# Optimization experiments

Measured on AMD Instinct MI355X. Metric: run time of the kernel, lower is better.

Reference implementation:

```python
import jax, jax.numpy as jnp
import numpy as np

V = 32000   # vocab
D = 1024    # dim
H = 16      # query heads
HKV = 8     # kv heads (GQA)
DH = D // H # head dim = 64
L = 2       # layers
FF = 3584   # expert hidden dim
E = 8       # experts
K = 2       # top-k
EPS = 1e-5
BASE = 1000000.0
B, S = 1, 2048


def setup_inputs() -> dict:
    key = jax.random.key(0)
    ks = jax.random.split(key, 10)
    s = 0.02
    return {
        "x": jax.random.randint(ks[0], (B, S), 0, V, dtype=jnp.int64) if jax.config.jax_enable_x64 else jax.random.randint(ks[0], (B, S), 0, V),
        "emb": jax.random.normal(ks[1], (V, D), jnp.float32) * s,
        "ln_w": jnp.ones((L, D), jnp.float32),
        "ffln_w": jnp.ones((L, D), jnp.float32),
        "wq": jax.random.normal(ks[2], (L, D, H * DH), jnp.float32) * s,
        "wk": jax.random.normal(ks[3], (L, D, HKV * DH), jnp.float32) * s,
        "wv": jax.random.normal(ks[4], (L, D, HKV * DH), jnp.float32) * s,
        "wo": jax.random.normal(ks[5], (L, H * DH, D), jnp.float32) * s,
        "gate_w": jax.random.normal(ks[6], (L, E, D), jnp.float32) * s,
        "w1": jax.random.normal(ks[7], (L, E, FF, D), jnp.float32) * s,
        "w2": jax.random.normal(ks[8], (L, E, D, FF), jnp.float32) * s,
        "w3": jax.random.normal(ks[9], (L, E, FF, D), jnp.float32) * s,
        "dec_norm_w": jnp.ones((D,), jnp.float32),
    }


def rmsnorm(x, w):
    # LayerNormParameterized(use_mean=False, shift=False) == RMSNorm, pow in fp32
    xf = x.astype(jnp.float32)
    var = jnp.mean(xf * xf, axis=-1, keepdims=True)
    return ((xf * jax.lax.rsqrt(var + EPS)).astype(x.dtype)) * w


def rope(xh, pos):
    # interleaved (complex-pair) rotary embedding, xh: [B, S, h, DH]
    half = DH // 2
    freqs = 1.0 / (BASE ** (jnp.arange(0, half, dtype=jnp.float32) * 2.0 / DH))
    ang = pos[:, None] * freqs[None, :]                       # [S, half]
    cos = jnp.cos(ang)[None, :, None, :]
    sin = jnp.sin(ang)[None, :, None, :]
    x1 = xh[..., 0::2]
    x2 = xh[..., 1::2]
    out = jnp.stack([x1 * cos - x2 * sin, x1 * sin + x2 * cos], axis=-1)
    return out.reshape(xh.shape)


def reference(x, emb, ln_w, ffln_w, wq, wk, wv, wo, gate_w, w1, w2, w3, dec_norm_w):
    h = emb[x]                                                # [B, S, D]
    pos = jnp.arange(S, dtype=jnp.float32)
    causal = jnp.tril(jnp.ones((S, S), bool))[None, None]     # [1,1,S,S]
    scale = 1.0 / np.sqrt(DH).astype(np.float32)
    for i in range(L):
        # --- attention sub-layer ---
        res = h
        xn = rmsnorm(h, ln_w[i])
        q = rope((xn @ wq[i]).reshape(B, S, H, DH), pos)
        k = rope((xn @ wk[i]).reshape(B, S, HKV, DH), pos)
        v = (xn @ wv[i]).reshape(B, S, HKV, DH)
        rep = H // HKV
        k = jnp.repeat(k, rep, axis=2)                        # [B,S,H,DH]
        v = jnp.repeat(v, rep, axis=2)
        scores = jnp.einsum('bqhd,bkhd->bhqk', q, k) * scale
        scores = jnp.where(causal, scores, jnp.float32(-1e9))
        att = jax.nn.softmax(scores, axis=-1)
        o = jnp.einsum('bhqk,bkhd->bqhd', att, v).reshape(B, S, H * DH) @ wo[i]
        h = res + o
        # --- MoE FFN sub-layer ---
        res = h
        xn = rmsnorm(h, ffln_w[i]).reshape(B * S, D)          # [T, D]
        logits = xn @ gate_w[i].T                             # [T, E]
        gates = jax.nn.softmax(logits, axis=-1)
        topw, topi = jax.lax.top_k(gates, K)                  # [T, K]
        topw = topw / jnp.sum(topw, axis=-1, keepdims=True)
        # dense combine weights [T, E] (zero for unselected experts)
        cw = jnp.einsum('tk,tke->te', topw, jax.nn.one_hot(topi, E, dtype=topw.dtype))
        y = jnp.zeros_like(xn)
        for e in range(E):                                    # fixed small expert loop
            ye = (jax.nn.silu(xn @ w1[i, e].T) * (xn @ w3[i, e].T)) @ w2[i, e].T
            y = y + cw[:, e:e + 1] * ye
        h = res + y.reshape(B, S, D)
    return rmsnorm(h, dec_norm_w)
```

## Files before the change

### kernel.cpp

```cpp
#include <hip/hip_runtime.h>

using u16 = unsigned short;
using u32 = unsigned int;

#define TT 2048
#define DM 1024
#define NH 16
#define NKV 8
#define DHD 64
#define FFD 3584
#define NE 8

typedef __bf16 bf16x8 __attribute__((ext_vector_type(8)));
typedef float f32x4 __attribute__((ext_vector_type(4)));

__device__ __forceinline__ u16 f2bf(float x){
  return __builtin_bit_cast(u16, (__bf16)x);
}
__device__ __forceinline__ float bf2f(u16 h){
  return (float)__builtin_bit_cast(__bf16, h);
}
__device__ __forceinline__ f32x4 mfma16(bf16x8 a, bf16x8 b, f32x4 c){
  return __builtin_amdgcn_mfma_f32_16x16x32_bf16(a, b, c, 0, 0, 0);
}
__device__ __forceinline__ uint4 packhi8v(float4 a, float4 b){
  u16 h0=f2bf(a.x),h1=f2bf(a.y),h2=f2bf(a.z),h3=f2bf(a.w);
  u16 h4=f2bf(b.x),h5=f2bf(b.y),h6=f2bf(b.z),h7=f2bf(b.w);
  return make_uint4((u32)h0|((u32)h1<<16),(u32)h2|((u32)h3<<16),
                    (u32)h4|((u32)h5<<16),(u32)h6|((u32)h7<<16));
}
__device__ __forceinline__ uint4 packlo8v(float4 a, float4 b){
  u16 l0=f2bf(a.x-bf2f(f2bf(a.x))),l1=f2bf(a.y-bf2f(f2bf(a.y)));
  u16 l2=f2bf(a.z-bf2f(f2bf(a.z))),l3=f2bf(a.w-bf2f(f2bf(a.w)));
  u16 l4=f2bf(b.x-bf2f(f2bf(b.x))),l5=f2bf(b.y-bf2f(f2bf(b.y)));
  u16 l6=f2bf(b.z-bf2f(f2bf(b.z))),l7=f2bf(b.w-bf2f(f2bf(b.w)));
  return make_uint4((u32)l0|((u32)l1<<16),(u32)l2|((u32)l3<<16),
                    (u32)l4|((u32)l5<<16),(u32)l6|((u32)l7<<16));
}

#define SWC(r,c) ((((c) ^ ((((r)>>1) ^ ((r)>>3)) & 3))) * 8)

__global__ __launch_bounds__(256) void k_embed(const int* __restrict__ x,
    const float* __restrict__ emb, float* __restrict__ h){
  int t = blockIdx.x;
  int d = threadIdx.x * 4;
  float4 v = *reinterpret_cast<const float4*>(emb + (size_t)x[t] * DM + d);
  *reinterpret_cast<float4*>(h + (size_t)t * DM + d) = v;
}

template<int OUTF32>
__global__ __launch_bounds__(256) void k_rmsnorm(const float* __restrict__ in,
    const float* __restrict__ w, u16* __restrict__ oh, u16* __restrict__ ol,
    float* __restrict__ of){
  int t = blockIdx.x;
  int d4 = threadIdx.x * 4;
  float4 xv = *reinterpret_cast<const float4*>(in + (size_t)t * DM + d4);
  float ss = xv.x*xv.x + xv.y*xv.y + xv.z*xv.z + xv.w*xv.w;
#pragma unroll
  for (int m = 1; m < 64; m <<= 1) ss += __shfl_xor(ss, m);
  __shared__ float sred[4];
  if ((threadIdx.x & 63) == 0) sred[threadIdx.x >> 6] = ss;
  __syncthreads();
  float tot = sred[0] + sred[1] + sred[2] + sred[3];
  float r = 1.0f / sqrtf(tot * (1.0f / DM) + 1e-5f);
  float vv[4] = {xv.x, xv.y, xv.z, xv.w};
#pragma unroll
  for (int jj = 0; jj < 4; jj++){
    float xn = (vv[jj] * r) * w[d4 + jj];
    size_t a = (size_t)t * DM + d4 + jj;
    if constexpr (OUTF32){
      of[a] = xn;
    } else {
      u16 hi = f2bf(xn);
      oh[a] = hi;
      ol[a] = f2bf(xn - bf2f(hi));
    }
  }
}

template<int NHD>
__global__ __launch_bounds__(256) void k_rope(const float* __restrict__ in,
    u16* __restrict__ oh, u16* __restrict__ ol){
  int idx = blockIdx.x * 256 + threadIdx.x;
  int j = idx & 31;
  int hd = (idx >> 5) % NHD;
  int s = idx / (32 * NHD);
  size_t base = ((size_t)s * NHD + hd) * 64 + 2 * j;
  float x1 = in[base], x2 = in[base + 1];
  float xe = (float)j * 0.03125f;
  float yf = (float)pow(1.0e6, (double)xe);
  float fr = 1.0f / yf;
  float ang = (float)s * fr;
  double ad = (double)ang;
  float c  = (float)cos(ad);
  float sn = (float)sin(ad);
  float o1 = x1 * c - x2 * sn;
  float o2 = x1 * sn + x2 * c;
  u16 h1 = f2bf(o1), h2 = f2bf(o2);
  oh[base]     = h1; ol[base]     = f2bf(o1 - bf2f(h1));
  oh[base + 1] = h2; ol[base + 1] = f2bf(o2 - bf2f(h2));
}

__global__ __launch_bounds__(256) void k_splitbuf(const float* __restrict__ in,
    u16* __restrict__ oh, u16* __restrict__ ol, int n){
  int i = blockIdx.x * 256 + threadIdx.x;
  if (i < n){
    float x = in[i];
    u16 hi = f2bf(x);
    oh[i] = hi;
    ol[i] = f2bf(x - bf2f(hi));
  }
}

__global__ __launch_bounds__(256) void k_gate(const u16* __restrict__ xh,
    const u16* __restrict__ xl, const float* __restrict__ gw,
    int* __restrict__ topi, float* __restrict__ topw, int* __restrict__ cnt){
  int wv = threadIdx.x >> 6, lane = threadIdx.x & 63;
  int t = blockIdx.x * 4 + wv;
  float x[16];
#pragma unroll
  for (int i = 0; i < 16; i++){
    size_t a = (size_t)t * DM + lane + 64 * i;
    x[i] = bf2f(xh[a]) + bf2f(xl[a]);
  }
  float lgt[8];
#pragma unroll
  for (int e = 0; e < 8; e++){
    float s = 0.f;
#pragma unroll
    for (int i = 0; i < 16; i++) s += x[i] * gw[(size_t)e * DM + lane + 64 * i];
#pragma unroll
    for (int m = 1; m < 64; m <<= 1) s += __shfl_xor(s, m);
    lgt[e] = s;
  }
  float mx = lgt[0];
#pragma unroll
  for (int e = 1; e < 8; e++) mx = fmaxf(mx, lgt[e]);
  float p[8]; float sum = 0.f;
#pragma unroll
  for (int e = 0; e < 8; e++){ p[e] = expf(lgt[e] - mx); sum += p[e]; }
  float g[8];
#pragma unroll
  for (int e = 0; e < 8; e++) g[e] = p[e] / sum;
  int t0 = 0; float b0 = g[0];
#pragma unroll
  for (int e = 1; e < 8; e++) if (g[e] > b0){ b0 = g[e]; t0 = e; }
  int t1 = -1; float b1 = -1.f;
#pragma unroll
  for (int e = 0; e < 8; e++) if (e != t0 && g[e] > b1){ b1 = g[e]; t1 = e; }
  float ssum = b0 + b1;
  float w0 = b0 / ssum, w1 = b1 / ssum;
  if (lane == 0 && t < TT){
    topi[2*t] = t0; topi[2*t+1] = t1;
    topw[2*t] = w0; topw[2*t+1] = w1;
    atomicAdd(&cnt[t0], 1);
    atomicAdd(&cnt[t1], 1);
  }
}

__global__ void k_zero8(int* cnt){ if (threadIdx.x < 8) cnt[threadIdx.x] = 0; }

__global__ void k_scan(const int* __restrict__ cnt, int* __restrict__ offp, int* __restrict__ cur){
  if (threadIdx.x == 0){
    int r = 0;
    for (int e = 0; e < 8; e++){ offp[e] = r; r += cnt[e]; }
  }
  if (threadIdx.x < 8) cur[threadIdx.x] = 0;
}

__global__ __launch_bounds__(256) void k_scatter(const int* __restrict__ topi,
    const float* __restrict__ topw, const int* __restrict__ offp, int* __restrict__ cur,
    int* __restrict__ ftok, float* __restrict__ fwt){
  int t = blockIdx.x * 256 + threadIdx.x;
  if (t < TT){
#pragma unroll
    for (int j = 0; j < 2; j++){
      int e = topi[2*t + j];
      int p = atomicAdd(&cur[e], 1);
      ftok[offp[e] + p] = t;
      fwt[offp[e] + p] = topw[2*t + j];
    }
  }
}

#define GPRELOAD(KK) do { \
    pAh0 = *reinterpret_cast<const uint4*>(Ah + arowA0 + (KK)); \
    pAh1 = *reinterpret_cast<const uint4*>(Ah + arowA1 + (KK)); \
    if constexpr (SPLIT){ \
      pAl0 = *reinterpret_cast<const uint4*>(Al + arowA0 + (KK)); \
      pAl1 = *reinterpret_cast<const uint4*>(Al + arowA1 + (KK)); \
    } \
    if constexpr (BLAYOUT == 0){ \
      const float* bp_ = Bw + (size_t)(n0 + br0) * K + (KK) + cb8; \
      pB0 = *reinterpret_cast<const float4*>(bp_); \
      pB1 = *reinterpret_cast<const float4*>(bp_ + 4); \
      if constexpr (TN == 128){ \
        const float* bp2_ = Bw + (size_t)(n0 + br1) * K + (KK) + cb8; \
        pB2 = *reinterpret_cast<const float4*>(bp2_); \
        pB3 = *reinterpret_cast<const float4*>(bp2_ + 4); \
      } \
      if constexpr (DUAL){ \
        const float* bq_ = B3w + (size_t)(n0 + br0) * K + (KK) + cb8; \
        pB2 = *reinterpret_cast<const float4*>(bq_); \
        pB3 = *reinterpret_cast<const float4*>(bq_ + 4); \
      } \
    } else { \
      pB0 = *reinterpret_cast<const float4*>(Bw + (size_t)((KK) + kk1) * Nq + n0 + nn1); \
      pB1 = *reinterpret_cast<const float4*>(Bw + (size_t)((KK) + 16 + kk1) * Nq + n0 + nn1); \
    } \
  } while(0)

template<int BLAYOUT, int EPI, int SPLIT, int DUAL, int TN, int KS>
__global__ __launch_bounds__(256) void k_gemm(
    const u16* __restrict__ Ah, const u16* __restrict__ Al,
    const float* __restrict__ Bw, const float* __restrict__ B3w,
    const float* __restrict__ Bw2, const float* __restrict__ Bw3,
    size_t strideB, int N, int K,
    float* __restrict__ Cf, int ldc,
    float* __restrict__ Cf2, float* __restrict__ Cf3,
    u16* __restrict__ Ch, u16* __restrict__ Cl,
    const int* __restrict__ cntp, const int* __restrict__ offp,
    const int* __restrict__ ftok, const float* __restrict__ fwt)
{
  static_assert(!(DUAL && TN != 64), "DUAL uses TN=64");
  static_assert(!(BLAYOUT == 1 && TN != 64), "BLAYOUT=1 uses TN=64");
  int cnt = TT, off = 0, ks = 0;
  if constexpr (EPI == 2 || EPI == 3){
    int e = blockIdx.z / KS;
    ks = blockIdx.z % KS;
    cnt = cntp[e]; off = offp[e];
    if ((int)blockIdx.y * 128 >= cnt) return;
    Bw += (size_t)e * strideB;
    if constexpr (DUAL) B3w += (size_t)e * strideB;
  } else if constexpr (KS > 1){
    ks = blockIdx.z;
  }
  __shared__ u16 Ash[128][32];
  __shared__ u16 Asl[SPLIT ? 128 : 1][32];
  __shared__ u16 Bh1[TN][32];
  __shared__ u16 Bl1[SPLIT ? TN : 1][32];
  __shared__ u16 Bh3[DUAL ? TN : 1][32];
  __shared__ u16 Bl3[(DUAL && SPLIT) ? TN : 1][32];

  const int tid = threadIdx.x;
  const int m0 = blockIdx.y * 128;

  int n0, Nq = N, ldq = ldc;
  float* Cq = Cf;
  if constexpr (EPI == 4){
    int bx = blockIdx.x;
    if (bx < 16){       n0 = bx * 64;        Nq = 1024; ldq = 1024; Cq = Cf;  }
    else if (bx < 24){  n0 = (bx - 16) * 64; Nq = 512;  ldq = 512;  Cq = Cf2; Bw = Bw2; }
    else {              n0 = (bx - 24) * 64; Nq = 512;  ldq = 512;  Cq = Cf3; Bw = Bw3; }
  } else {
    n0 = blockIdx.x * TN;
  }

  const int r0 = tid >> 2;
  const int r1 = r0 + 64;
  const int ca = tid & 3;
  const int ca8 = ca * 8;
  int gr0, gr1;
  {
    int g0 = m0 + r0, g1 = m0 + r1;
    if constexpr (EPI == 2){
      gr0 = ftok[off + (g0 < cnt ? g0 : cnt - 1)];
      gr1 = ftok[off + (g1 < cnt ? g1 : cnt - 1)];
    } else if constexpr (EPI == 3){
      gr0 = off + (g0 < cnt ? g0 : cnt - 1);
      gr1 = off + (g1 < cnt ? g1 : cnt - 1);
    } else {
      gr0 = g0; gr1 = g1;
    }
  }
  const size_t arowA0 = (size_t)gr0 * K + ca8;
  const size_t arowA1 = (size_t)gr1 * K + ca8;
  const int swA0 = SWC(r0, ca), swA1 = SWC(r1, ca);

  const int br0 = tid >> 2;
  const int br1 = br0 + 64;
  const int cb8 = (tid & 3) * 8;
  const int swB0 = SWC(br0, tid & 3), swB1 = SWC(br1, tid & 3);
  const int kk1 = tid >> 4;
  const int nn1 = (tid & 15) * 4;

  const int wid = tid >> 6, lane = tid & 63;
  const int wr = wid >> 1, wc = wid & 1;
  const int lr = lane & 15, lg = lane >> 4;
  constexpr int NF = TN / 32;

  f32x4 acc[4][NF];
  f32x4 acc3[DUAL ? 4 : 1][NF];
#pragma unroll
  for (int m = 0; m < 4; m++)
#pragma unroll
    for (int n = 0; n < NF; n++){
      acc[m][n] = f32x4{0.f,0.f,0.f,0.f};
      if constexpr (DUAL) acc3[m][n] = f32x4{0.f,0.f,0.f,0.f};
    }

  uint4 pAh0, pAh1, pAl0{}, pAl1{};
  float4 pB0{}, pB1{}, pB2{}, pB3{};

  const int kbeg = ks * (K / KS);
  const int kend = kbeg + (K / KS);

  GPRELOAD(kbeg);
  for (int k0 = kbeg; k0 < kend; k0 += 32){
    *reinterpret_cast<uint4*>(&Ash[r0][swA0]) = pAh0;
    *reinterpret_cast<uint4*>(&Ash[r1][swA1]) = pAh1;
    if constexpr (SPLIT){
      *reinterpret_cast<uint4*>(&Asl[r0][swA0]) = pAl0;
      *reinterpret_cast<uint4*>(&Asl[r1][swA1]) = pAl1;
    }
    if constexpr (BLAYOUT == 0){
      *reinterpret_cast<uint4*>(&Bh1[br0][swB0]) = packhi8v(pB0, pB1);
      if constexpr (SPLIT) *reinterpret_cast<uint4*>(&Bl1[br0][swB0]) = packlo8v(pB0, pB1);
      if constexpr (TN == 128){
        *reinterpret_cast<uint4*>(&Bh1[br1][swB1]) = packhi8v(pB2, pB3);
        if constexpr (SPLIT) *reinterpret_cast<uint4*>(&Bl1[br1][swB1]) = packlo8v(pB2, pB3);
      }
      if constexpr (DUAL){
        *reinterpret_cast<uint4*>(&Bh3[br0][swB0]) = packhi8v(pB2, pB3);
        if constexpr (SPLIT) *reinterpret_cast<uint4*>(&Bl3[br0][swB0]) = packlo8v(pB2, pB3);
      }
    } else {
      const float* q0 = reinterpret_cast<const float*>(&pB0);
      const float* q1 = reinterpret_cast<const float*>(&pB1);
      const int ch0 = kk1 >> 3, off0 = kk1 & 7;
#pragma unroll
      for (int j = 0; j < 4; j++){
        int row = nn1 + j;
        int c0 = SWC(row, ch0) + off0;
        int c1 = SWC(row, ch0 + 2) + off0;
        u16 h0 = f2bf(q0[j]);
        Bh1[row][c0] = h0;
        if constexpr (SPLIT) Bl1[row][c0] = f2bf(q0[j] - bf2f(h0));
        u16 h1 = f2bf(q1[j]);
        Bh1[row][c1] = h1;
        if constexpr (SPLIT) Bl1[row][c1] = f2bf(q1[j] - bf2f(h1));
      }
    }
    __syncthreads();
    if (k0 + 32 < kend){ GPRELOAD(k0 + 32); }

    bf16x8 af[4], afl[4];
#pragma unroll
    for (int m = 0; m < 4; m++){
      int Ra = wr*64 + m*16 + lr;
      int sa = SWC(Ra, lg);
      af[m] = *reinterpret_cast<const bf16x8*>(&Ash[Ra][sa]);
      if constexpr (SPLIT)
        afl[m] = *reinterpret_cast<const bf16x8*>(&Asl[Ra][sa]);
    }
#pragma unroll
    for (int n = 0; n < NF; n++){
      int Rb = wc*(TN/2) + n*16 + lr;
      int sb = SWC(Rb, lg);
      bf16x8 b1 = *reinterpret_cast<const bf16x8*>(&Bh1[Rb][sb]);
#pragma unroll
      for (int m = 0; m < 4; m++) acc[m][n] = mfma16(af[m], b1, acc[m][n]);
      if constexpr (SPLIT){
        bf16x8 bl = *reinterpret_cast<const bf16x8*>(&Bl1[Rb][sb]);
#pragma unroll
        for (int m = 0; m < 4; m++){
          acc[m][n] = mfma16(af[m], bl, acc[m][n]);
          acc[m][n] = mfma16(afl[m], b1, acc[m][n]);
        }
      }
      if constexpr (DUAL){
        bf16x8 b3 = *reinterpret_cast<const bf16x8*>(&Bh3[Rb][sb]);
#pragma unroll
        for (int m = 0; m < 4; m++) acc3[m][n] = mfma16(af[m], b3, acc3[m][n]);
        if constexpr (SPLIT){
          bf16x8 b3l = *reinterpret_cast<const bf16x8*>(&Bl3[Rb][sb]);
#pragma unroll
          for (int m = 0; m < 4; m++){
            acc3[m][n] = mfma16(af[m], b3l, acc3[m][n]);
            acc3[m][n] = mfma16(afl[m], b3, acc3[m][n]);
          }
        }
      }
    }
    __syncthreads();
  }

#pragma unroll
  for (int m = 0; m < 4; m++)
#pragma unroll
    for (int n = 0; n < NF; n++)
#pragma unroll
      for (int r = 0; r < 4; r++){
        int row = m0 + wr*64 + m*16 + lg*4 + r;
        int col = n0 + wc*(TN/2) + n*16 + lr;
        float v = acc[m][n][r];
        if constexpr (EPI == 0){
          Cf[(size_t)row * ldc + col] = v;
        } else if constexpr (EPI == 1){
          if constexpr (KS > 1) atomicAdd(&Cf[(size_t)row * ldc + col], v);
          else                  Cf[(size_t)row * ldc + col] += v;
        } else if constexpr (EPI == 2){
          if (row < cnt){
            float a3 = acc3[m][n][r];
            float s = v / (1.0f + expf(-v));
            float y = s * a3;
            u16 hi = f2bf(y);
            size_t oa = (size_t)(off + row) * ldc + col;
            Ch[oa] = hi;
            Cl[oa] = f2bf(y - bf2f(hi));
          }
        } else if constexpr (EPI == 3){
          if (row < cnt){
            int tok = ftok[off + row];
            float wgt = fwt[off + row];
            atomicAdd(&Cf[(size_t)tok * ldc + col], wgt * v);
          }
        } else {
          if constexpr (KS > 1) atomicAdd(&Cq[(size_t)row * ldq + col], v);
          else                  Cq[(size_t)row * ldq + col] = v;
        }
      }
}

__global__ __launch_bounds__(256) void k_attn(
    const u16* __restrict__ qh, const u16* __restrict__ ql,
    const u16* __restrict__ kh, const u16* __restrict__ kl,
    const u16* __restrict__ vh, const u16* __restrict__ vl,
    u16* __restrict__ aoh, u16* __restrict__ aol)
{
  const int h  = blockIdx.y;
  const int q0 = blockIdx.x * 64;
  const int hk = h >> 1;
  const int tid = threadIdx.x;
  const int wv = tid >> 6, lane = tid & 63;
  const int lr = lane & 15, lg = lane >> 4;
  const int qw0 = q0 + wv * 16;

  __shared__ u16 Khs[32][72], Kls[32][72];
  __shared__ u16 Vhs[64][40], Vls[64][40];
  __shared__ u16 Phs[4][16][40], Pls[4][16][40];

  bf16x8 qfh[2], qfl[2];
#pragma unroll
  for (int dc = 0; dc < 2; dc++){
    size_t qa = ((size_t)(qw0 + lr) * NH + h) * 64 + dc*32 + lg*8;
    qfh[dc] = *reinterpret_cast<const bf16x8*>(qh + qa);
    qfl[dc] = *reinterpret_cast<const bf16x8*>(ql + qa);
  }
  f32x4 oacc[4];
  float mrun[4], lrun[4];
#pragma unroll
  for (int r = 0; r < 4; r++){ mrun[r] = -1e30f; lrun[r] = 0.f; }
#pragma unroll
  for (int g = 0; g < 4; g++) oacc[g] = f32x4{0.f,0.f,0.f,0.f};

  const int nt = q0 / 32 + 2;
  for (int kt = 0; kt < nt; kt++){
    int kg = kt * 32;
    {
      int kk = tid >> 3, c8 = (tid & 7) * 8;
      size_t ka = ((size_t)(kg + kk) * NKV + hk) * 64 + c8;
      *reinterpret_cast<uint4*>(&Khs[kk][c8]) = *reinterpret_cast<const uint4*>(kh + ka);
      *reinterpret_cast<uint4*>(&Kls[kk][c8]) = *reinterpret_cast<const uint4*>(kl + ka);
      uint4 v1 = *reinterpret_cast<const uint4*>(vh + ka);
      uint4 v2 = *reinterpret_cast<const uint4*>(vl + ka);
      const u16* p1 = reinterpret_cast<const u16*>(&v1);
      const u16* p2 = reinterpret_cast<const u16*>(&v2);
#pragma unroll
      for (int j = 0; j < 8; j++){ Vhs[c8 + j][kk] = p1[j]; Vls[c8 + j][kk] = p2[j]; }
    }
    __syncthreads();

    f32x4 sc[2];
    sc[0] = f32x4{0.f,0.f,0.f,0.f};
    sc[1] = f32x4{0.f,0.f,0.f,0.f};
#pragma unroll
    for (int c = 0; c < 2; c++){
#pragma unroll
      for (int dc = 0; dc < 2; dc++){
        bf16x8 bh = *reinterpret_cast<const bf16x8*>(&Khs[c*16 + lr][dc*32 + lg*8]);
        bf16x8 bl = *reinterpret_cast<const bf16x8*>(&Kls[c*16 + lr][dc*32 + lg*8]);
        sc[c] = mfma16(qfh[dc], bh, sc[c]);
        sc[c] = mfma16(qfh[dc], bl, sc[c]);
        sc[c] = mfma16(qfl[dc], bh, sc[c]);
      }
    }
    float pnew[2][4], corr[4];
#pragma unroll
    for (int r = 0; r < 4; r++){
      int row = qw0 + lg*4 + r;
      float s0 = (kg + lr      <= row) ? sc[0][r] * 0.125f : -1e30f;
      float s1 = (kg + 16 + lr <= row) ? sc[1][r] * 0.125f : -1e30f;
      float tm = fmaxf(s0, s1);
#pragma unroll
      for (int m = 1; m < 16; m <<= 1) tm = fmaxf(tm, __shfl_xor(tm, m));
      float mnew = fmaxf(mrun[r], tm);
      corr[r] = expf(mrun[r] - mnew);
      float p0 = expf(s0 - mnew);
      float p1 = expf(s1 - mnew);
      pnew[0][r] = p0; pnew[1][r] = p1;
      float sm = p0 + p1;
#pragma unroll
      for (int m = 1; m < 16; m <<= 1) sm += __shfl_xor(sm, m);
      lrun[r] = lrun[r] * corr[r] + sm;
      mrun[r] = mnew;
    }
#pragma unroll
    for (int g = 0; g < 4; g++){
      f32x4 t = oacc[g];
#pragma unroll
      for (int r = 0; r < 4; r++) t[r] *= corr[r];
      oacc[g] = t;
    }
#pragma unroll
    for (int c = 0; c < 2; c++)
#pragma unroll
      for (int r = 0; r < 4; r++){
        float p = pnew[c][r];
        u16 hi = f2bf(p);
        Phs[wv][lg*4 + r][c*16 + lr] = hi;
        Pls[wv][lg*4 + r][c*16 + lr] = f2bf(p - bf2f(hi));
      }
    asm volatile("s_waitcnt lgkmcnt(0)" ::: "memory");
    __builtin_amdgcn_sched_barrier(0);
    bf16x8 pah = *reinterpret_cast<const bf16x8*>(&Phs[wv][lr][lg*8]);
    bf16x8 pal = *reinterpret_cast<const bf16x8*>(&Pls[wv][lr][lg*8]);
#pragma unroll
    for (int g = 0; g < 4; g++){
      bf16x8 vb1 = *reinterpret_cast<const bf16x8*>(&Vhs[g*16 + lr][lg*8]);
      bf16x8 vb2 = *reinterpret_cast<const bf16x8*>(&Vls[g*16 + lr][lg*8]);
      oacc[g] = mfma16(pah, vb1, oacc[g]);
      oacc[g] = mfma16(pah, vb2, oacc[g]);
      oacc[g] = mfma16(pal, vb1, oacc[g]);
    }
    __syncthreads();
  }
#pragma unroll
  for (int g = 0; g < 4; g++)
#pragma unroll
    for (int r = 0; r < 4; r++){
      int row = qw0 + lg*4 + r;
      float v = oacc[g][r] / lrun[r];
      u16 hi = f2bf(v);
      size_t oa = ((size_t)row * NH + h) * 64 + g*16 + lr;
      aoh[oa] = hi;
      aol[oa] = f2bf(v - bf2f(hi));
    }
}

extern "C" void kernel_launch(void* const* d_in, const int* in_sizes, int n_in,
                              void* d_out, int out_size, void* d_ws, size_t ws_size,
                              hipStream_t stream){
  const int*   x     = (const int*)d_in[0];
  const float* emb   = (const float*)d_in[1];
  const float* lnw   = (const float*)d_in[2];
  const float* fflnw = (const float*)d_in[3];
  const float* wq    = (const float*)d_in[4];
  const float* wk    = (const float*)d_in[5];
  const float* wvp   = (const float*)d_in[6];
  const float* wo    = (const float*)d_in[7];
  const float* gw    = (const float*)d_in[8];
  const float* w1    = (const float*)d_in[9];
  const float* w2    = (const float*)d_in[10];
  const float* w3    = (const float*)d_in[11];
  const float* dnw   = (const float*)d_in[12];
  float* out = (float*)d_out;

  char* p = (char*)d_ws;
  auto alloc = [&](size_t bytes)->char*{
    char* r = p; p += (bytes + 255) & ~(size_t)255; return r;
  };
  float* h    = (float*)alloc((size_t)TT * DM * 4);
  float* qbuf = (float*)alloc((size_t)TT * 1024 * 4);
  float* kbuf = (float*)alloc((size_t)TT * 512 * 4);
  float* vbuf = (float*)alloc((size_t)TT * 512 * 4);
  u16* xnh = (u16*)alloc((size_t)TT * DM * 2);
  u16* xnl = (u16*)alloc((size_t)TT * DM * 2);
  u16* qhb = (u16*)alloc((size_t)TT * 1024 * 2);
  u16* qlb = (u16*)alloc((size_t)TT * 1024 * 2);
  u16* khb = (u16*)alloc((size_t)TT * 512 * 2);
  u16* klb = (u16*)alloc((size_t)TT * 512 * 2);
  u16* vhb = (u16*)alloc((size_t)TT * 512 * 2);
  u16* vlb = (u16*)alloc((size_t)TT * 512 * 2);
  u16* aoh = (u16*)alloc((size_t)TT * 1024 * 2);
  u16* aol = (u16*)alloc((size_t)TT * 1024 * 2);
  u16* acth = (u16*)alloc((size_t)2 * TT * FFD * 2);
  u16* actl = (u16*)alloc((size_t)2 * TT * FFD * 2);
  int*   topi = (int*)alloc((size_t)2 * TT * 4);
  float* topw = (float*)alloc((size_t)2 * TT * 4);
  int* cnt  = (int*)alloc(64);
  int* offe = (int*)alloc(64);
  int* cur  = (int*)alloc(64);
  int*   ftok = (int*)alloc((size_t)2 * TT * 4);
  float* fwt  = (float*)alloc((size_t)2 * TT * 4);

  k_embed<<<TT, 256, 0, stream>>>(x, emb, h);

  for (int i = 0; i < 2; i++){
    const float* wq_i = wq + (size_t)i * DM * 1024;
    const float* wk_i = wk + (size_t)i * DM * 512;
    const float* wv_i = wvp + (size_t)i * DM * 512;
    const float* wo_i = wo + (size_t)i * 1024 * DM;
    const float* w1_i = w1 + (size_t)i * NE * FFD * DM;
    const float* w2_i = w2 + (size_t)i * NE * DM * FFD;
    const float* w3_i = w3 + (size_t)i * NE * FFD * DM;

    k_rmsnorm<0><<<TT, 256, 0, stream>>>(h, lnw + i * DM, xnh, xnl, nullptr);

    hipMemsetAsync(qbuf, 0, (size_t)TT * 1024 * 4, stream);
    hipMemsetAsync(kbuf, 0, (size_t)TT * 512 * 4, stream);
    hipMemsetAsync(vbuf, 0, (size_t)TT * 512 * 4, stream);
    k_gemm<1,4,1,0,64,2><<<dim3(32,16,2), 256, 0, stream>>>(xnh, xnl,
        wq_i, nullptr, wk_i, wv_i, 0, 1024, DM,
        qbuf, 1024, kbuf, vbuf, nullptr, nullptr, nullptr, nullptr, nullptr, nullptr);

    k_rope<16><<<4096, 256, 0, stream>>>(qbuf, qhb, qlb);
    k_rope<8><<<2048, 256, 0, stream>>>(kbuf, khb, klb);
    k_splitbuf<<<4096, 256, 0, stream>>>(vbuf, vhb, vlb, TT * 512);

    k_attn<<<dim3(32,16,1), 256, 0, stream>>>(qhb, qlb, khb, klb, vhb, vlb, aoh, aol);

    k_gemm<1,1,1,0,64,2><<<dim3(16,16,2), 256, 0, stream>>>(aoh, aol,
        wo_i, nullptr, nullptr, nullptr, 0, DM, 1024,
        h, DM, nullptr, nullptr, nullptr, nullptr, nullptr, nullptr, nullptr, nullptr);

    k_rmsnorm<0><<<TT, 256, 0, stream>>>(h, fflnw + i * DM, xnh, xnl, nullptr);

    k_zero8<<<1, 64, 0, stream>>>(cnt);
    k_gate<<<TT/4, 256, 0, stream>>>(xnh, xnl, gw + (size_t)i * NE * DM, topi, topw, cnt);
    k_scan<<<1, 64, 0, stream>>>(cnt, offe, cur);
    k_scatter<<<8, 256, 0, stream>>>(topi, topw, offe, cur, ftok, fwt);

    if (i == 0){
      k_gemm<0,2,1,1,64,1><<<dim3(FFD/64,16,8), 256, 0, stream>>>(xnh, xnl,
          w1_i, w3_i, nullptr, nullptr, (size_t)FFD * DM, FFD, DM,
          nullptr, FFD, nullptr, nullptr, acth, actl, cnt, offe, ftok, fwt);
      k_gemm<0,3,1,0,128,4><<<dim3(DM/128,16,32), 256, 0, stream>>>(acth, actl,
          w2_i, nullptr, nullptr, nullptr, (size_t)DM * FFD, DM, FFD,
          h, DM, nullptr, nullptr, nullptr, nullptr, cnt, offe, ftok, fwt);
    } else {
      k_gemm<0,2,0,1,64,1><<<dim3(FFD/64,16,8), 256, 0, stream>>>(xnh, xnl,
          w1_i, w3_i, nullptr, nullptr, (size_t)FFD * DM, FFD, DM,
          nullptr, FFD, nullptr, nullptr, acth, actl, cnt, offe, ftok, fwt);
      k_gemm<0,3,0,0,128,4><<<dim3(DM/128,16,32), 256, 0, stream>>>(acth, actl,
          w2_i, nullptr, nullptr, nullptr, (size_t)DM * FFD, DM, FFD,
          h, DM, nullptr, nullptr, nullptr, nullptr, cnt, offe, ftok, fwt);
    }
  }

  k_rmsnorm<1><<<TT, 256, 0, stream>>>(h, dnw, nullptr, nullptr, out);
}
```

Before: 1.530 ms.

## Deepen GEMM global-load prefetch to two register stages

The GEMM main loop now keeps two sets of prefetch registers and alternates between them. This lets global loads for the K-tile two steps ahead be issued while the current tile is computed, which is meant to hide more global memory latency. The cost is higher register pressure, which could lower occupancy or cause spills. The loop also steps by 64 and so assumes each split's K range is a multiple of 64.

Measured after the change: 1.677 ms. 1.1x slower.

```diff
diff --git a/kernel.cpp b/kernel.cpp
--- a/kernel.cpp
+++ b/kernel.cpp
@@ -183,30 +183,108 @@
   }
 }
 
-#define GPRELOAD(KK) do { \
-    pAh0 = *reinterpret_cast<const uint4*>(Ah + arowA0 + (KK)); \
-    pAh1 = *reinterpret_cast<const uint4*>(Ah + arowA1 + (KK)); \
+#define GPRELOAD(S, KK) do { \
+    S##Ah0 = *reinterpret_cast<const uint4*>(Ah + arowA0 + (KK)); \
+    S##Ah1 = *reinterpret_cast<const uint4*>(Ah + arowA1 + (KK)); \
     if constexpr (SPLIT){ \
-      pAl0 = *reinterpret_cast<const uint4*>(Al + arowA0 + (KK)); \
-      pAl1 = *reinterpret_cast<const uint4*>(Al + arowA1 + (KK)); \
+      S##Al0 = *reinterpret_cast<const uint4*>(Al + arowA0 + (KK)); \
+      S##Al1 = *reinterpret_cast<const uint4*>(Al + arowA1 + (KK)); \
     } \
     if constexpr (BLAYOUT == 0){ \
       const float* bp_ = Bw + (size_t)(n0 + br0) * K + (KK) + cb8; \
-      pB0 = *reinterpret_cast<const float4*>(bp_); \
-      pB1 = *reinterpret_cast<const float4*>(bp_ + 4); \
+      S##B0 = *reinterpret_cast<const float4*>(bp_); \
+      S##B1 = *reinterpret_cast<const float4*>(bp_ + 4); \
       if constexpr (TN == 128){ \
         const float* bp2_ = Bw + (size_t)(n0 + br1) * K + (KK) + cb8; \
-        pB2 = *reinterpret_cast<const float4*>(bp2_); \
-        pB3 = *reinterpret_cast<const float4*>(bp2_ + 4); \
+        S##B2 = *reinterpret_cast<const float4*>(bp2_); \
+        S##B3 = *reinterpret_cast<const float4*>(bp2_ + 4); \
       } \
       if constexpr (DUAL){ \
         const float* bq_ = B3w + (size_t)(n0 + br0) * K + (KK) + cb8; \
-        pB2 = *reinterpret_cast<const float4*>(bq_); \
-        pB3 = *reinterpret_cast<const float4*>(bq_ + 4); \
+        S##B2 = *reinterpret_cast<const float4*>(bq_); \
+        S##B3 = *reinterpret_cast<const float4*>(bq_ + 4); \
       } \
     } else { \
-      pB0 = *reinterpret_cast<const float4*>(Bw + (size_t)((KK) + kk1) * Nq + n0 + nn1); \
-      pB1 = *reinterpret_cast<const float4*>(Bw + (size_t)((KK) + 16 + kk1) * Nq + n0 + nn1); \
+      S##B0 = *reinterpret_cast<const float4*>(Bw + (size_t)((KK) + kk1) * Nq + n0 + nn1); \
+      S##B1 = *reinterpret_cast<const float4*>(Bw + (size_t)((KK) + 16 + kk1) * Nq + n0 + nn1); \
+    } \
+  } while(0)
+
+#define GSTORE(S) do { \
+    *reinterpret_cast<uint4*>(&Ash[r0][swA0]) = S##Ah0; \
+    *reinterpret_cast<uint4*>(&Ash[r1][swA1]) = S##Ah1; \
+    if constexpr (SPLIT){ \
+      *reinterpret_cast<uint4*>(&Asl[r0][swA0]) = S##Al0; \
+      *reinterpret_cast<uint4*>(&Asl[r1][swA1]) = S##Al1; \
+    } \
+    if constexpr (BLAYOUT == 0){ \
+      *reinterpret_cast<uint4*>(&Bh1[br0][swB0]) = packhi8v(S##B0, S##B1); \
+      if constexpr (SPLIT) *reinterpret_cast<uint4*>(&Bl1[br0][swB0]) = packlo8v(S##B0, S##B1); \
+      if constexpr (TN == 128){ \
+        *reinterpret_cast<uint4*>(&Bh1[br1][swB1]) = packhi8v(S##B2, S##B3); \
+        if constexpr (SPLIT) *reinterpret_cast<uint4*>(&Bl1[br1][swB1]) = packlo8v(S##B2, S##B3); \
+      } \
+      if constexpr (DUAL){ \
+        *reinterpret_cast<uint4*>(&Bh3[br0][swB0]) = packhi8v(S##B2, S##B3); \
+        if constexpr (SPLIT) *reinterpret_cast<uint4*>(&Bl3[br0][swB0]) = packlo8v(S##B2, S##B3); \
+      } \
+    } else { \
+      const float* q0 = reinterpret_cast<const float*>(&S##B0); \
+      const float* q1 = reinterpret_cast<const float*>(&S##B1); \
+      const int ch0 = kk1 >> 3, off0 = kk1 & 7; \
+      _Pragma("unroll") \
+      for (int j = 0; j < 4; j++){ \
+        int row = nn1 + j; \
+        int c0 = SWC(row, ch0) + off0; \
+        int c1 = SWC(row, ch0 + 2) + off0; \
+        u16 h0 = f2bf(q0[j]); \
+        Bh1[row][c0] = h0; \
+        if constexpr (SPLIT) Bl1[row][c0] = f2bf(q0[j] - bf2f(h0)); \
+        u16 h1 = f2bf(q1[j]); \
+        Bh1[row][c1] = h1; \
+        if constexpr (SPLIT) Bl1[row][c1] = f2bf(q1[j] - bf2f(h1)); \
+      } \
+    } \
+  } while(0)
+
+#define MFMA_PHASE() do { \
+    bf16x8 af[4], afl[4]; \
+    _Pragma("unroll") \
+    for (int m = 0; m < 4; m++){ \
+      int Ra = wr*64 + m*16 + lr; \
+      int sa = SWC(Ra, lg); \
+      af[m] = *reinterpret_cast<const bf16x8*>(&Ash[Ra][sa]); \
+      if constexpr (SPLIT) \
+        afl[m] = *reinterpret_cast<const bf16x8*>(&Asl[Ra][sa]); \
+    } \
+    _Pragma("unroll") \
+    for (int n = 0; n < NF; n++){ \
+      int Rb = wc*(TN/2) + n*16 + lr; \
+      int sb = SWC(Rb, lg); \
+      bf16x8 b1 = *reinterpret_cast<const bf16x8*>(&Bh1[Rb][sb]); \
+      _Pragma("unroll") \
+      for (int m = 0; m < 4; m++) acc[m][n] = mfma16(af[m], b1, acc[m][n]); \
+      if constexpr (SPLIT){ \
+        bf16x8 bl = *reinterpret_cast<const bf16x8*>(&Bl1[Rb][sb]); \
+        _Pragma("unroll") \
+        for (int m = 0; m < 4; m++){ \
+          acc[m][n] = mfma16(af[m], bl, acc[m][n]); \
+          acc[m][n] = mfma16(afl[m], b1, acc[m][n]); \
+        } \
+      } \
+      if constexpr (DUAL){ \
+        bf16x8 b3 = *reinterpret_cast<const bf16x8*>(&Bh3[Rb][sb]); \
+        _Pragma("unroll") \
+        for (int m = 0; m < 4; m++) acc3[m][n] = mfma16(af[m], b3, acc3[m][n]); \
+        if constexpr (SPLIT){ \
+          bf16x8 b3l = *reinterpret_cast<const bf16x8*>(&Bl3[Rb][sb]); \
+          _Pragma("unroll") \
+          for (int m = 0; m < 4; m++){ \
+            acc3[m][n] = mfma16(af[m], b3l, acc3[m][n]); \
+            acc3[m][n] = mfma16(afl[m], b3, acc3[m][n]); \
+          } \
+        } \
+      } \
     } \
   } while(0)
 
@@ -299,89 +377,27 @@
       if constexpr (DUAL) acc3[m][n] = f32x4{0.f,0.f,0.f,0.f};
     }
 
-  uint4 pAh0, pAh1, pAl0{}, pAl1{};
-  float4 pB0{}, pB1{}, pB2{}, pB3{};
+  uint4 aAh0, aAh1, aAl0{}, aAl1{};
+  float4 aB0{}, aB1{}, aB2{}, aB3{};
+  uint4 bAh0, bAh1, bAl0{}, bAl1{};
+  float4 bB0{}, bB1{}, bB2{}, bB3{};
 
   const int kbeg = ks * (K / KS);
   const int kend = kbeg + (K / KS);
 
-  GPRELOAD(kbeg);
-  for (int k0 = kbeg; k0 < kend; k0 += 32){
-    *reinterpret_cast<uint4*>(&Ash[r0][swA0]) = pAh0;
-    *reinterpret_cast<uint4*>(&Ash[r1][swA1]) = pAh1;
-    if constexpr (SPLIT){
-      *reinterpret_cast<uint4*>(&Asl[r0][swA0]) = pAl0;
-      *reinterpret_cast<uint4*>(&Asl[r1][swA1]) = pAl1;
-    }
-    if constexpr (BLAYOUT == 0){
-      *reinterpret_cast<uint4*>(&Bh1[br0][swB0]) = packhi8v(pB0, pB1);
-      if constexpr (SPLIT) *reinterpret_cast<uint4*>(&Bl1[br0][swB0]) = packlo8v(pB0, pB1);
-      if constexpr (TN == 128){
-        *reinterpret_cast<uint4*>(&Bh1[br1][swB1]) = packhi8v(pB2, pB3);
-        if constexpr (SPLIT) *reinterpret_cast<uint4*>(&Bl1[br1][swB1]) = packlo8v(pB2, pB3);
-      }
-      if constexpr (DUAL){
-        *reinterpret_cast<uint4*>(&Bh3[br0][swB0]) = packhi8v(pB2, pB3);
-        if constexpr (SPLIT) *reinterpret_cast<uint4*>(&Bl3[br0][swB0]) = packlo8v(pB2, pB3);
-      }
-    } else {
-      const float* q0 = reinterpret_cast<const float*>(&pB0);
-      const float* q1 = reinterpret_cast<const float*>(&pB1);
-      const int ch0 = kk1 >> 3, off0 = kk1 & 7;
-#pragma unroll
-      for (int j = 0; j < 4; j++){
-        int row = nn1 + j;
-        int c0 = SWC(row, ch0) + off0;
-        int c1 = SWC(row, ch0 + 2) + off0;
-        u16 h0 = f2bf(q0[j]);
-        Bh1[row][c0] = h0;
-        if constexpr (SPLIT) Bl1[row][c0] = f2bf(q0[j] - bf2f(h0));
-        u16 h1 = f2bf(q1[j]);
-        Bh1[row][c1] = h1;
-        if constexpr (SPLIT) Bl1[row][c1] = f2bf(q1[j] - bf2f(h1));
-      }
-    }
+  GPRELOAD(a, kbeg);
+  GPRELOAD(b, kbeg + 32);
+  for (int k0 = kbeg; k0 < kend; k0 += 64){
+    GSTORE(a);
     __syncthreads();
-    if (k0 + 32 < kend){ GPRELOAD(k0 + 32); }
-
-    bf16x8 af[4], afl[4];
-#pragma unroll
-    for (int m = 0; m < 4; m++){
-      int Ra = wr*64 + m*16 + lr;
-      int sa = SWC(Ra, lg);
-      af[m] = *reinterpret_cast<const bf16x8*>(&Ash[Ra][sa]);
-      if constexpr (SPLIT)
-        afl[m] = *reinterpret_cast<const bf16x8*>(&Asl[Ra][sa]);
-    }
-#pragma unroll
-    for (int n = 0; n < NF; n++){
-      int Rb = wc*(TN/2) + n*16 + lr;
-      int sb = SWC(Rb, lg);
-      bf16x8 b1 = *reinterpret_cast<const bf16x8*>(&Bh1[Rb][sb]);
-#pragma unroll
-      for (int m = 0; m < 4; m++) acc[m][n] = mfma16(af[m], b1, acc[m][n]);
-      if constexpr (SPLIT){
-        bf16x8 bl = *reinterpret_cast<const bf16x8*>(&Bl1[Rb][sb]);
-#pragma unroll
-        for (int m = 0; m < 4; m++){
-          acc[m][n] = mfma16(af[m], bl, acc[m][n]);
-          acc[m][n] = mfma16(afl[m], b1, acc[m][n]);
-        }
-      }
-      if constexpr (DUAL){
-        bf16x8 b3 = *reinterpret_cast<const bf16x8*>(&Bh3[Rb][sb]);
-#pragma unroll
-        for (int m = 0; m < 4; m++) acc3[m][n] = mfma16(af[m], b3, acc3[m][n]);
-        if constexpr (SPLIT){
-          bf16x8 b3l = *reinterpret_cast<const bf16x8*>(&Bl3[Rb][sb]);
-#pragma unroll
-          for (int m = 0; m < 4; m++){
-            acc3[m][n] = mfma16(af[m], b3l, acc3[m][n]);
-            acc3[m][n] = mfma16(afl[m], b3, acc3[m][n]);
-          }
-        }
-      }
-    }
+    if (k0 + 64 < kend){ GPRELOAD(a, k0 + 64); }
+    MFMA_PHASE();
+    __syncthreads();
+
+    GSTORE(b);
+    __syncthreads();
+    if (k0 + 96 < kend){ GPRELOAD(b, k0 + 96); }
+    MFMA_PHASE();
     __syncthreads();
   }
 
```
